# Performance work log

Hardware: AMD Instinct MI355X
Metric: run time of the kernel (lower is better)

The kernel has to match this reference:

```python
import jax, jax.numpy as jnp
import numpy as np

B, L, D, V = 64, 512, 768, 100
LN_EPS = 1e-6


def setup_inputs() -> dict:
    key = jax.random.key(0)
    k1, k2, k3, k4 = jax.random.split(key, 4)
    return {
        "ids": jax.random.randint(k1, (B, 1), 0, V),
        "pooler": jax.random.normal(k2, (B, L, D), dtype=jnp.float32),
        "emb_table": jax.random.normal(k3, (V, 2), dtype=jnp.float32),
        "W_dense": jax.random.normal(k4, (2, D), dtype=jnp.float32) * 0.1,
        "b_dense": jnp.zeros((D,), dtype=jnp.float32),
        "gamma": jnp.ones((D,), dtype=jnp.float32),
        "beta": jnp.zeros((D,), dtype=jnp.float32),
    }


def reference(ids, pooler, emb_table, W_dense, b_dense, gamma, beta):
    # id -> 2-dim projection -> dense to embed_dim: xt (B, 1, D)
    emb = emb_table[ids]                      # (B, 1, 2)
    xt = emb @ W_dense + b_dense              # (B, 1, D)

    # Per timestep i the original concatenates [pooler[:, i], xt] into a
    # 2-token sequence and runs dot-product self-attention (keras Attention,
    # no scaling), then sums over the 2 tokens. Vectorized over all L steps:
    tok = jnp.stack([pooler, jnp.broadcast_to(xt, pooler.shape)], axis=2)  # (B, L, 2, D)
    scores = jnp.einsum('blqd,blkd->blqk', tok, tok)                       # (B, L, 2, 2)
    attn = jax.nn.softmax(scores, axis=-1)
    out = jnp.einsum('blqk,blkd->blqd', attn, tok)                         # (B, L, 2, D)
    summed = out.sum(axis=2)                                               # (B, L, D)

    # dropout is identity at inference; layernorm over last axis, eps=1e-6
    mean = summed.mean(axis=-1, keepdims=True)
    var = summed.var(axis=-1, keepdims=True)
    normed = (summed - mean) * jax.lax.rsqrt(var + LN_EPS)
    return normed * gamma + beta
```

## Files before the change

### kernel.cpp

```cpp
#include <hip/hip_runtime.h>


constexpr int Bc = 64;
constexpr int Lc = 512;
constexpr int Dc = 768;
constexpr int NF4 = Dc / 4;
constexpr float LN_EPS = 1e-6f;
constexpr int WPB = 4;
constexpr int RPW = 2;
constexpr int RPB = WPB * RPW;

typedef float nv_float4 __attribute__((ext_vector_type(4)));

__global__ __launch_bounds__(64 * WPB) void hier_attn_ln_kernel(
    const int*   __restrict__ ids,
    const float* __restrict__ pooler,
    const float* __restrict__ emb_table,
    const float* __restrict__ W,
    const float* __restrict__ bvec,
    const float* __restrict__ gamma,
    const float* __restrict__ beta,
    float*       __restrict__ out)
{
    __shared__ float4 tile[WPB][RPW][NF4];

    const int wave = threadIdx.x >> 6;
    const int lane = threadIdx.x & 63;
    const int row0 = blockIdx.x * RPB + wave * RPW;
    const int b    = row0 >> 9;

    const float4* W0_4 = (const float4*)W;
    const float4* W1_4 = (const float4*)(W + Dc);
    const float4* b_4  = (const float4*)bvec;
    const float4* g_4  = (const float4*)gamma;
    const float4* be_4 = (const float4*)beta;

    const int id = ids[b];
    const float e0 = emb_table[id * 2 + 0];
    const float e1 = emb_table[id * 2 + 1];

    float4 xt[3];
    float s11 = 0.f, S1 = 0.f;
#pragma unroll
    for (int j = 0; j < 3; ++j) {
        const int i4 = lane + j * 64;
        float4 w0 = W0_4[i4], w1 = W1_4[i4], bd = b_4[i4];
        float4 x;
        x.x = fmaf(e0, w0.x, fmaf(e1, w1.x, bd.x));
        x.y = fmaf(e0, w0.y, fmaf(e1, w1.y, bd.y));
        x.z = fmaf(e0, w0.z, fmaf(e1, w1.z, bd.z));
        x.w = fmaf(e0, w0.w, fmaf(e1, w1.w, bd.w));
        xt[j] = x;
        s11 += x.x*x.x + x.y*x.y + x.z*x.z + x.w*x.w;
        S1  += x.x + x.y + x.z + x.w;
    }

    const float4* p_base = (const float4*)(pooler + (size_t)row0 * Dc);
    float s00[RPW], s01[RPW], S0[RPW];
#pragma unroll
    for (int r = 0; r < RPW; ++r) {
        float a0 = 0.f, a1 = 0.f, a2 = 0.f;
#pragma unroll
        for (int j = 0; j < 3; ++j) {
            const int i4 = lane + j * 64;
            const float4 p = p_base[r * NF4 + i4];
            tile[wave][r][i4] = p;
            a0 += p.x*p.x + p.y*p.y + p.z*p.z + p.w*p.w;
            a1 += p.x*xt[j].x + p.y*xt[j].y + p.z*xt[j].z + p.w*xt[j].w;
            a2 += p.x + p.y + p.z + p.w;
        }
        s00[r] = a0; s01[r] = a1; S0[r] = a2;
    }

#pragma unroll
    for (int off = 32; off > 0; off >>= 1) {
        s11 += __shfl_xor(s11, off);
        S1  += __shfl_xor(S1,  off);
#pragma unroll
        for (int r = 0; r < RPW; ++r) {
            s00[r] += __shfl_xor(s00[r], off);
            s01[r] += __shfl_xor(s01[r], off);
            S0[r]  += __shfl_xor(S0[r],  off);
        }
    }

    float4 gm[3], bt[3];
#pragma unroll
    for (int j = 0; j < 3; ++j) {
        gm[j] = g_4[lane + j * 64];
        bt[j] = be_4[lane + j * 64];
    }

    const float invD = 1.f / (float)Dc;
    float ascale[RPW], cscale[RPW], mshift[RPW];
#pragma unroll
    for (int r = 0; r < RPW; ++r) {
        const float m0  = fmaxf(s00[r], s01[r]);
        const float a00 = __expf(s00[r] - m0);
        const float a01 = __expf(s01[r] - m0);
        const float r0  = 1.f / (a00 + a01);
        const float m1  = fmaxf(s01[r], s11);
        const float a10 = __expf(s01[r] - m1);
        const float a11 = __expf(s11 - m1);
        const float r1  = 1.f / (a10 + a11);
        const float w0s = a00 * r0 + a10 * r1;
        const float w1s = a01 * r0 + a11 * r1;

        const float mean = (w0s * S0[r] + w1s * S1) * invD;
        const float ex2  = (w0s*w0s*s00[r] + 2.f*w0s*w1s*s01[r] + w1s*w1s*s11) * invD;
        const float var  = ex2 - mean * mean;
        const float rstd = rsqrtf(var + LN_EPS);

        ascale[r] = w0s * rstd;
        cscale[r] = w1s * rstd;
        mshift[r] = mean * rstd;
    }

    nv_float4* o_base = (nv_float4*)(out + (size_t)row0 * Dc);
#pragma unroll
    for (int r = 0; r < RPW; ++r) {
        const float a = ascale[r], c = cscale[r], m = mshift[r];
        nv_float4* orow = o_base + (size_t)r * NF4;
#pragma unroll
        for (int j = 0; j < 3; ++j) {
            const int i4 = lane + j * 64;
            const float4 p = tile[wave][r][i4];
            nv_float4 o;
            o.x = fmaf(gm[j].x, fmaf(a, p.x, fmaf(c, xt[j].x, -m)), bt[j].x);
            o.y = fmaf(gm[j].y, fmaf(a, p.y, fmaf(c, xt[j].y, -m)), bt[j].y);
            o.z = fmaf(gm[j].z, fmaf(a, p.z, fmaf(c, xt[j].z, -m)), bt[j].z);
            o.w = fmaf(gm[j].w, fmaf(a, p.w, fmaf(c, xt[j].w, -m)), bt[j].w);
            __builtin_nontemporal_store(o, &orow[i4]);
        }
    }
}

extern "C" void kernel_launch(void* const* d_in, const int* in_sizes, int n_in,
                              void* d_out, int out_size, void* d_ws, size_t ws_size,
                              hipStream_t stream) {
    const int*   ids       = (const int*)  d_in[0];
    const float* pooler    = (const float*)d_in[1];
    const float* emb_table = (const float*)d_in[2];
    const float* W_dense   = (const float*)d_in[3];
    const float* b_dense   = (const float*)d_in[4];
    const float* gamma     = (const float*)d_in[5];
    const float* beta      = (const float*)d_in[6];
    float* out = (float*)d_out;

    const int nrows = Bc * Lc;
    hipLaunchKernelGGL(hier_attn_ln_kernel,
                       dim3(nrows / RPB), dim3(64 * WPB),
                       0, stream,
                       ids, pooler, emb_table, W_dense, b_dense, gamma, beta, out);
}
```

Before: 187.3 us.

## Software-pipeline rows per wave in registers, dropping the shared-memory tile

Each wave now processes eight rows in a software-pipelined loop. It loads the next row's pooler data into registers while it writes the previous row's normalized output, and keeps the current row in registers instead of staging it in LDS. Gamma and beta loads move up front, and the launch bounds request 4 blocks per SM. This removes the LDS round-trip and amortizes the per-wave setup (xt, gamma, beta) over more rows. In exchange there are fewer blocks in the grid (1024) and less memory-level parallelism per wave, since only one row is in flight at a time.

```diff
diff --git a/kernel.cpp b/kernel.cpp
--- a/kernel.cpp
+++ b/kernel.cpp
@@ -7,12 +7,12 @@
 constexpr int NF4 = Dc / 4;
 constexpr float LN_EPS = 1e-6f;
 constexpr int WPB = 4;
-constexpr int RPW = 2;
+constexpr int RPW = 8;
 constexpr int RPB = WPB * RPW;
 
 typedef float nv_float4 __attribute__((ext_vector_type(4)));
 
-__global__ __launch_bounds__(64 * WPB) void hier_attn_ln_kernel(
+__global__ __launch_bounds__(64 * WPB, 4) void hier_attn_ln_kernel(
     const int*   __restrict__ ids,
     const float* __restrict__ pooler,
     const float* __restrict__ emb_table,
@@ -22,11 +22,10 @@
     const float* __restrict__ beta,
     float*       __restrict__ out)
 {
-    __shared__ float4 tile[WPB][RPW][NF4];
-
     const int wave = threadIdx.x >> 6;
     const int lane = threadIdx.x & 63;
-    const int row0 = blockIdx.x * RPB + wave * RPW;
+    const int wid  = blockIdx.x * WPB + wave;
+    const int row0 = wid * RPW;
     const int b    = row0 >> 9;
 
     const float4* W0_4 = (const float4*)W;
@@ -39,12 +38,14 @@
     const float e0 = emb_table[id * 2 + 0];
     const float e1 = emb_table[id * 2 + 1];
 
-    float4 xt[3];
+    float4 xt[3], gm[3], bt[3];
     float s11 = 0.f, S1 = 0.f;
 #pragma unroll
     for (int j = 0; j < 3; ++j) {
         const int i4 = lane + j * 64;
         float4 w0 = W0_4[i4], w1 = W1_4[i4], bd = b_4[i4];
+        gm[j] = g_4[i4];
+        bt[j] = be_4[i4];
         float4 x;
         x.x = fmaf(e0, w0.x, fmaf(e1, w1.x, bd.x));
         x.y = fmaf(e0, w0.y, fmaf(e1, w1.y, bd.y));
@@ -54,83 +55,118 @@
         s11 += x.x*x.x + x.y*x.y + x.z*x.z + x.w*x.w;
         S1  += x.x + x.y + x.z + x.w;
     }
-
-    const float4* p_base = (const float4*)(pooler + (size_t)row0 * Dc);
-    float s00[RPW], s01[RPW], S0[RPW];
-#pragma unroll
-    for (int r = 0; r < RPW; ++r) {
-        float a0 = 0.f, a1 = 0.f, a2 = 0.f;
-#pragma unroll
-        for (int j = 0; j < 3; ++j) {
-            const int i4 = lane + j * 64;
-            const float4 p = p_base[r * NF4 + i4];
-            tile[wave][r][i4] = p;
-            a0 += p.x*p.x + p.y*p.y + p.z*p.z + p.w*p.w;
-            a1 += p.x*xt[j].x + p.y*xt[j].y + p.z*xt[j].z + p.w*xt[j].w;
-            a2 += p.x + p.y + p.z + p.w;
-        }
-        s00[r] = a0; s01[r] = a1; S0[r] = a2;
-    }
-
 #pragma unroll
     for (int off = 32; off > 0; off >>= 1) {
         s11 += __shfl_xor(s11, off);
         S1  += __shfl_xor(S1,  off);
-#pragma unroll
-        for (int r = 0; r < RPW; ++r) {
-            s00[r] += __shfl_xor(s00[r], off);
-            s01[r] += __shfl_xor(s01[r], off);
-            S0[r]  += __shfl_xor(S0[r],  off);
-        }
-    }
-
-    float4 gm[3], bt[3];
-#pragma unroll
-    for (int j = 0; j < 3; ++j) {
-        gm[j] = g_4[lane + j * 64];
-        bt[j] = be_4[lane + j * 64];
     }
 
     const float invD = 1.f / (float)Dc;
-    float ascale[RPW], cscale[RPW], mshift[RPW];
+    const float4* p_base = (const float4*)(pooler + (size_t)row0 * Dc);
+    nv_float4*    o_base = (nv_float4*)(out + (size_t)row0 * Dc);
+
+    float4 pp[3];
+    float pa, pc, pm;
+
+    {
+        float a0 = 0.f, a1 = 0.f, a2 = 0.f;
 #pragma unroll
-    for (int r = 0; r < RPW; ++r) {
-        const float m0  = fmaxf(s00[r], s01[r]);
-        const float a00 = __expf(s00[r] - m0);
-        const float a01 = __expf(s01[r] - m0);
-        const float r0  = 1.f / (a00 + a01);
-        const float m1  = fmaxf(s01[r], s11);
-        const float a10 = __expf(s01[r] - m1);
-        const float a11 = __expf(s11 - m1);
-        const float r1  = 1.f / (a10 + a11);
-        const float w0s = a00 * r0 + a10 * r1;
-        const float w1s = a01 * r0 + a11 * r1;
-
-        const float mean = (w0s * S0[r] + w1s * S1) * invD;
-        const float ex2  = (w0s*w0s*s00[r] + 2.f*w0s*w1s*s01[r] + w1s*w1s*s11) * invD;
-        const float var  = ex2 - mean * mean;
-        const float rstd = rsqrtf(var + LN_EPS);
-
-        ascale[r] = w0s * rstd;
-        cscale[r] = w1s * rstd;
-        mshift[r] = mean * rstd;
+        for (int j = 0; j < 3; ++j) {
+            const float4 q = p_base[lane + j * 64];
+            pp[j] = q;
+            a0 += q.x*q.x + q.y*q.y + q.z*q.z + q.w*q.w;
+            a1 += q.x*xt[j].x + q.y*xt[j].y + q.z*xt[j].z + q.w*xt[j].w;
+            a2 += q.x + q.y + q.z + q.w;
+        }
+#pragma unroll
+        for (int off = 32; off > 0; off >>= 1) {
+            a0 += __shfl_xor(a0, off);
+            a1 += __shfl_xor(a1, off);
+            a2 += __shfl_xor(a2, off);
+        }
+        const float m0  = fmaxf(a0, a1);
+        const float x00 = __expf(a0 - m0);
+        const float x01 = __expf(a1 - m0);
+        const float r0  = 1.f / (x00 + x01);
+        const float m1  = fmaxf(a1, s11);
+        const float x10 = __expf(a1 - m1);
+        const float x11 = __expf(s11 - m1);
+        const float r1  = 1.f / (x10 + x11);
+        const float w0s = x00 * r0 + x10 * r1;
+        const float w1s = x01 * r0 + x11 * r1;
+        const float mean = (w0s * a2 + w1s * S1) * invD;
+        const float ex2  = (w0s*w0s*a0 + 2.f*w0s*w1s*a1 + w1s*w1s*s11) * invD;
+        const float rstd = rsqrtf(ex2 - mean * mean + LN_EPS);
+        pa = w0s * rstd; pc = w1s * rstd; pm = mean * rstd;
     }
 
-    nv_float4* o_base = (nv_float4*)(out + (size_t)row0 * Dc);
+#pragma unroll 1
+    for (int r = 1; r < RPW; ++r) {
+        const float4 q0 = p_base[r * NF4 + lane];
+        const float4 q1 = p_base[r * NF4 + lane + 64];
+        const float4 q2 = p_base[r * NF4 + lane + 128];
+
+        {
+            nv_float4* orow = o_base + (size_t)(r - 1) * NF4;
 #pragma unroll
-    for (int r = 0; r < RPW; ++r) {
-        const float a = ascale[r], c = cscale[r], m = mshift[r];
-        nv_float4* orow = o_base + (size_t)r * NF4;
+            for (int j = 0; j < 3; ++j) {
+                const float4 p = pp[j];
+                nv_float4 o;
+                o.x = fmaf(gm[j].x, fmaf(pa, p.x, fmaf(pc, xt[j].x, -pm)), bt[j].x);
+                o.y = fmaf(gm[j].y, fmaf(pa, p.y, fmaf(pc, xt[j].y, -pm)), bt[j].y);
+                o.z = fmaf(gm[j].z, fmaf(pa, p.z, fmaf(pc, xt[j].z, -pm)), bt[j].z);
+                o.w = fmaf(gm[j].w, fmaf(pa, p.w, fmaf(pc, xt[j].w, -pm)), bt[j].w);
+                __builtin_nontemporal_store(o, &orow[lane + j * 64]);
+            }
+        }
+
+        float a0, a1, a2;
+        {
+            a0  = q0.x*q0.x + q0.y*q0.y + q0.z*q0.z + q0.w*q0.w;
+            a1  = q0.x*xt[0].x + q0.y*xt[0].y + q0.z*xt[0].z + q0.w*xt[0].w;
+            a2  = q0.x + q0.y + q0.z + q0.w;
+            a0 += q1.x*q1.x + q1.y*q1.y + q1.z*q1.z + q1.w*q1.w;
+            a1 += q1.x*xt[1].x + q1.y*xt[1].y + q1.z*xt[1].z + q1.w*xt[1].w;
+            a2 += q1.x + q1.y + q1.z + q1.w;
+            a0 += q2.x*q2.x + q2.y*q2.y + q2.z*q2.z + q2.w*q2.w;
+            a1 += q2.x*xt[2].x + q2.y*xt[2].y + q2.z*xt[2].z + q2.w*xt[2].w;
+            a2 += q2.x + q2.y + q2.z + q2.w;
+            pp[0] = q0; pp[1] = q1; pp[2] = q2;
+        }
+
+#pragma unroll
+        for (int off = 32; off > 0; off >>= 1) {
+            a0 += __shfl_xor(a0, off);
+            a1 += __shfl_xor(a1, off);
+            a2 += __shfl_xor(a2, off);
+        }
+        const float m0  = fmaxf(a0, a1);
+        const float x00 = __expf(a0 - m0);
+        const float x01 = __expf(a1 - m0);
+        const float r0  = 1.f / (x00 + x01);
+        const float m1  = fmaxf(a1, s11);
+        const float x10 = __expf(a1 - m1);
+        const float x11 = __expf(s11 - m1);
+        const float r1  = 1.f / (x10 + x11);
+        const float w0s = x00 * r0 + x10 * r1;
+        const float w1s = x01 * r0 + x11 * r1;
+        const float mean = (w0s * a2 + w1s * S1) * invD;
+        const float ex2  = (w0s*w0s*a0 + 2.f*w0s*w1s*a1 + w1s*w1s*s11) * invD;
+        const float rstd = rsqrtf(ex2 - mean * mean + LN_EPS);
+        pa = w0s * rstd; pc = w1s * rstd; pm = mean * rstd;
+    }
+
+    {
+        nv_float4* orow = o_base + (size_t)(RPW - 1) * NF4;
 #pragma unroll
         for (int j = 0; j < 3; ++j) {
-            const int i4 = lane + j * 64;
-            const float4 p = tile[wave][r][i4];
+            const float4 p = pp[j];
             nv_float4 o;
-            o.x = fmaf(gm[j].x, fmaf(a, p.x, fmaf(c, xt[j].x, -m)), bt[j].x);
-            o.y = fmaf(gm[j].y, fmaf(a, p.y, fmaf(c, xt[j].y, -m)), bt[j].y);
-            o.z = fmaf(gm[j].z, fmaf(a, p.z, fmaf(c, xt[j].z, -m)), bt[j].z);
-            o.w = fmaf(gm[j].w, fmaf(a, p.w, fmaf(c, xt[j].w, -m)), bt[j].w);
-            __builtin_nontemporal_store(o, &orow[i4]);
+            o.x = fmaf(gm[j].x, fmaf(pa, p.x, fmaf(pc, xt[j].x, -pm)), bt[j].x);
+            o.y = fmaf(gm[j].y, fmaf(pa, p.y, fmaf(pc, xt[j].y, -pm)), bt[j].y);
+            o.z = fmaf(gm[j].z, fmaf(pa, p.z, fmaf(pc, xt[j].z, -pm)), bt[j].z);
+            o.w = fmaf(gm[j].w, fmaf(pa, p.w, fmaf(pc, xt[j].w, -pm)), bt[j].w);
+            __builtin_nontemporal_store(o, &orow[lane + j * 64]);
         }
     }
 }
```

Result: slower. 194.0 us (+3.6%).
